# Performance work log

Hardware: AMD Instinct MI355X
Metric: run time of the kernel (lower is better)

## Reference

```python
import jax, jax.numpy as jnp
import numpy as np
import math

DIM = 1024; NH = 16; HD = 64; RANK = 512
E = 8; TOPK = 2; EH = 512
THETA = 10000.0; EPS = 1e-6
B = 2; T = 2048


def setup_inputs():
    key = jax.random.key(0)
    ks = jax.random.split(key, 12)
    s = 0.02
    return {
        "x": jax.random.normal(ks[0], (B, T, DIM), jnp.float32),
        "attn_norm_w": jnp.ones((DIM,), jnp.float32),
        "ffn_norm_w": jnp.ones((DIM,), jnp.float32),
        "q_norm_w": jnp.ones((HD,), jnp.float32),
        "k_norm_w": jnp.ones((HD,), jnp.float32),
        "wq": jax.random.normal(ks[1], (NH * HD, DIM), jnp.float32) * s,
        "wkv_down": jax.random.normal(ks[2], (RANK, DIM), jnp.float32) * s,
        "wkv_up": jax.random.normal(ks[3], (2 * NH * HD, RANK), jnp.float32) * s,
        "wo": jax.random.normal(ks[4], (DIM, NH * HD), jnp.float32) * s,
        "gate_w": jax.random.normal(ks[5], (E, DIM), jnp.float32) * s,
        "shared_w1": jax.random.normal(ks[6], (EH, DIM), jnp.float32) * s,
        "shared_w2": jax.random.normal(ks[7], (DIM, EH), jnp.float32) * s,
        "expert_w1": jax.random.normal(ks[8], (E, EH, DIM), jnp.float32) * s,
        "expert_w2": jax.random.normal(ks[9], (E, DIM, EH), jnp.float32) * s,
    }


def rmsnorm(x, w):
    var = jnp.mean(x * x, axis=-1, keepdims=True)
    return x * jax.lax.rsqrt(var + EPS) * w


def rope(x, cos, sin):
    # x: [B,T,H,HD]; pairs are (even, odd) along last dim. cos/sin: [T,1,HD//2]
    xr = x.reshape(*x.shape[:-1], HD // 2, 2)
    a, b = xr[..., 0], xr[..., 1]
    out = jnp.stack([a * cos - b * sin, a * sin + b * cos], axis=-1)
    return out.reshape(x.shape)


def _block(x, attn_norm_w, ffn_norm_w, q_norm_w, k_norm_w,
           wq, wkv_down, wkv_up, wo, gate_w,
           shared_w1, shared_w2, expert_w1, expert_w2):
    Bb, Tt, C = x.shape
    # ---- MLA attention ----
    h_in = rmsnorm(x, attn_norm_w)
    xq = jnp.einsum('btd,ed->bte', h_in, wq).reshape(Bb, Tt, NH, HD)
    latent = jnp.einsum('btd,rd->btr', h_in, wkv_down)
    kv = jnp.einsum('btr,er->bte', latent, wkv_up).reshape(Bb, Tt, 2, NH, HD)
    xk, xv = kv[:, :, 0], kv[:, :, 1]
    xq = rmsnorm(xq, q_norm_w)
    xk = rmsnorm(xk, k_norm_w)
    # RoPE tables
    inv = 1.0 / (THETA ** (jnp.arange(0, HD, 2, dtype=jnp.float32) / HD))  # [HD/2]
    ang = jnp.arange(Tt, dtype=jnp.float32)[:, None] * inv[None, :]       # [T,HD/2]
    cos = jnp.cos(ang)[:, None, :]
    sin = jnp.sin(ang)[:, None, :]
    xq = rope(xq, cos, sin)
    xk = rope(xk, cos, sin)
    scale = 1.0 / math.sqrt(HD)
    scores = jnp.einsum('bqhd,bkhd->bhqk', xq, xk) * scale
    causal = jnp.tril(jnp.ones((Tt, Tt), dtype=bool))
    scores = jnp.where(causal, scores, jnp.finfo(scores.dtype).min)
    attn = jax.nn.softmax(scores, axis=-1)
    attn_out = jnp.einsum('bhqk,bkhd->bqhd', attn, xv).reshape(Bb, Tt, C)
    attn_out = jnp.einsum('bte,de->btd', attn_out, wo)
    h = x + attn_out  # dropout p=0.0 -> identity

    # ---- DeepSeekMoE ----
    xm = rmsnorm(h, ffn_norm_w).reshape(-1, C)  # [N,D]
    shared = jnp.einsum('nh,dh->nd', jax.nn.silu(jnp.einsum('nd,hd->nh', xm, shared_w1)), shared_w2)
    logits = jnp.einsum('nd,ed->ne', xm, gate_w)
    probs = jax.nn.softmax(logits, axis=-1)
    tkw, tki = jax.lax.top_k(probs, TOPK)
    tkw = tkw / jnp.sum(tkw, axis=-1, keepdims=True)
    aux_loss = jnp.sum(jnp.mean(probs, axis=0) * jnp.mean(logits, axis=0)) * E
    # combine weights per expert: [N,E]
    combine = jnp.einsum('nk,nke->ne', tkw, jax.nn.one_hot(tki, E, dtype=tkw.dtype))
    hidden = jax.nn.silu(jnp.einsum('nd,ehd->neh', xm, expert_w1))  # [N,E,EH]
    yexp = jnp.einsum('neh,edh->ned', hidden, expert_w2)            # [N,E,D]
    routed = jnp.einsum('ne,ned->nd', combine, yexp)
    moe_out = (shared + routed).reshape(Bb, Tt, C)
    out = h + moe_out
    return out, aux_loss


def reference(x, attn_norm_w, ffn_norm_w, q_norm_w, k_norm_w,
              wq, wkv_down, wkv_up, wo, gate_w,
              shared_w1, shared_w2, expert_w1, expert_w2):
    return _block(x, attn_norm_w, ffn_norm_w, q_norm_w, k_norm_w,
                  wq, wkv_down, wkv_up, wo, gate_w,
                  shared_w1, shared_w2, expert_w1, expert_w2)
```

## Files before the change

kernel.cpp:

```cpp
#include <hip/hip_runtime.h>
#include <math.h>

#define DIMC 1024
#define NHEADS 16
#define HDC 64
#define RANKC 512
#define NEXP 8
#define EHC 512
#define SEQC 2048
#define NBATCH 2
#define NTOK (NBATCH * SEQC)
#define EPSF 1e-6f

typedef unsigned short u16;
using bf16x8 = __attribute__((ext_vector_type(8))) short;
using f32x4 = __attribute__((ext_vector_type(4))) float;

__device__ inline u16 f2bf(float f) {
    unsigned int u = __float_as_uint(f);
    u += 0x7fff + ((u >> 16) & 1);
    return (u16)(u >> 16);
}
__device__ inline float bf2f(u16 u) { return __uint_as_float(((unsigned int)u) << 16); }

__device__ inline void gld16(const void* g, void* l) {
    __builtin_amdgcn_global_load_lds(
        (const __attribute__((address_space(1))) unsigned int*)g,
        (__attribute__((address_space(3))) unsigned int*)l, 16, 0, 0);
}

__global__ __launch_bounds__(256) void convall_k(
    const float* __restrict__ wq, const float* __restrict__ wkvd,
    const float* __restrict__ wkvu, const float* __restrict__ wo,
    const float* __restrict__ sw1, const float* __restrict__ sw2,
    const float* __restrict__ ew1, const float* __restrict__ ew2,
    u16* __restrict__ wqkvd_h, u16* __restrict__ wqkvd_l,
    u16* __restrict__ wkvu_h, u16* __restrict__ wkvu_l,
    u16* __restrict__ wo_h, u16* __restrict__ wo_l,
    u16* __restrict__ sw1_b, u16* __restrict__ sw2_b,
    u16* __restrict__ ew1_b, u16* __restrict__ ew2_b,
    const float* __restrict__ x, const float* __restrict__ attn_nw,
    u16* __restrict__ hin_h, u16* __restrict__ hin_l) {
    __shared__ float sred[4];
    if (blockIdx.x >= 12800) {
        int row = blockIdx.x - 12800;
        const float* xr = x + (size_t)row * DIMC;
        int base = threadIdx.x * 4;
        float4 xv = *(const float4*)(xr + base);
        float ss = xv.x * xv.x + xv.y * xv.y + xv.z * xv.z + xv.w * xv.w;
#pragma unroll
        for (int off = 32; off; off >>= 1) ss += __shfl_down(ss, off);
        int wid = threadIdx.x >> 6, lane = threadIdx.x & 63;
        if (lane == 0) sred[wid] = ss;
        __syncthreads();
        float tot = sred[0] + sred[1] + sred[2] + sred[3];
        float sc = rsqrtf(tot * (1.0f / DIMC) + EPSF);
        float4 wv = *(const float4*)(attn_nw + base);
        float o0 = xv.x * sc * wv.x, o1 = xv.y * sc * wv.y;
        float o2 = xv.z * sc * wv.z, o3 = xv.w * sc * wv.w;
        ushort4 h = make_ushort4(f2bf(o0), f2bf(o1), f2bf(o2), f2bf(o3));
        size_t ob = (size_t)row * DIMC + base;
        *(ushort4*)(hin_h + ob) = h;
        ushort4 lo = make_ushort4(f2bf(o0 - bf2f(h.x)), f2bf(o1 - bf2f(h.y)),
                                  f2bf(o2 - bf2f(h.z)), f2bf(o3 - bf2f(h.w)));
        *(ushort4*)(hin_l + ob) = lo;
        return;
    }
    size_t f = ((size_t)blockIdx.x * 256 + threadIdx.x) * 4;
    const float* src;
    u16* dh;
    u16* dl = nullptr;
    size_t local;
    if (f < 1048576) { src = wq; dh = wqkvd_h; dl = wqkvd_l; local = f; }
    else if (f < 1572864) { src = wkvd; dh = wqkvd_h + 1048576; dl = wqkvd_l + 1048576; local = f - 1048576; }
    else if (f < 2621440) { src = wkvu; dh = wkvu_h; dl = wkvu_l; local = f - 1572864; }
    else if (f < 3670016) { src = wo; dh = wo_h; dl = wo_l; local = f - 2621440; }
    else if (f < 4194304) { src = sw1; dh = sw1_b; local = f - 3670016; }
    else if (f < 4718592) { src = sw2; dh = sw2_b; local = f - 4194304; }
    else if (f < 8912896) { src = ew1; dh = ew1_b; local = f - 4718592; }
    else { src = ew2; dh = ew2_b; local = f - 8912896; }
    float4 a = *(const float4*)(src + local);
    ushort4 h = make_ushort4(f2bf(a.x), f2bf(a.y), f2bf(a.z), f2bf(a.w));
    *(ushort4*)(dh + local) = h;
    if (dl) {
        ushort4 lo = make_ushort4(f2bf(a.x - bf2f(h.x)), f2bf(a.y - bf2f(h.y)),
                                  f2bf(a.z - bf2f(h.z)), f2bf(a.w - bf2f(h.w)));
        *(ushort4*)(dl + local) = lo;
    }
}

__global__ __launch_bounds__(256) void rmsnorm_gate_k(const float* __restrict__ x,
                                                      const float* __restrict__ w,
                                                      u16* __restrict__ oh,
                                                      const float* __restrict__ gw,
                                                      float* __restrict__ topw,
                                                      int* __restrict__ topi,
                                                      float* __restrict__ plbuf) {
    int row = blockIdx.x;
    const float* xr = x + (size_t)row * DIMC;
    int base = threadIdx.x * 4;
    float4 xv = *(const float4*)(xr + base);
    float ss = xv.x * xv.x + xv.y * xv.y + xv.z * xv.z + xv.w * xv.w;
#pragma unroll
    for (int off = 32; off; off >>= 1) ss += __shfl_down(ss, off);
    __shared__ float sred[4];
    __shared__ float red[4][NEXP];
    int wid = threadIdx.x >> 6, lane = threadIdx.x & 63;
    if (lane == 0) sred[wid] = ss;
    __syncthreads();
    float tot = sred[0] + sred[1] + sred[2] + sred[3];
    float sc = rsqrtf(tot * (1.0f / DIMC) + EPSF);
    float4 wv = *(const float4*)(w + base);
    float o0 = xv.x * sc * wv.x, o1 = xv.y * sc * wv.y;
    float o2 = xv.z * sc * wv.z, o3 = xv.w * sc * wv.w;
    size_t ob = (size_t)row * DIMC + base;
    *(ushort4*)(oh + ob) = make_ushort4(f2bf(o0), f2bf(o1), f2bf(o2), f2bf(o3));
    float acc[NEXP];
#pragma unroll
    for (int e = 0; e < NEXP; e++) {
        float4 gv = *(const float4*)(gw + (size_t)e * DIMC + base);
        acc[e] = o0 * gv.x + o1 * gv.y + o2 * gv.z + o3 * gv.w;
    }
#pragma unroll
    for (int off = 32; off; off >>= 1)
#pragma unroll
        for (int e = 0; e < NEXP; e++) acc[e] += __shfl_down(acc[e], off);
    if (lane == 0)
#pragma unroll
        for (int e = 0; e < NEXP; e++) red[wid][e] = acc[e];
    __syncthreads();
    if (threadIdx.x == 0) {
        float lg[NEXP], p[NEXP];
        float mx = -1e30f;
#pragma unroll
        for (int e = 0; e < NEXP; e++) {
            lg[e] = red[0][e] + red[1][e] + red[2][e] + red[3][e];
            mx = fmaxf(mx, lg[e]);
        }
        float s = 0.f;
#pragma unroll
        for (int e = 0; e < NEXP; e++) { p[e] = __expf(lg[e] - mx); s += p[e]; }
        float invs = 1.0f / s;
#pragma unroll
        for (int e = 0; e < NEXP; e++) p[e] *= invs;
        int i0 = 0;
        for (int e = 1; e < NEXP; e++) if (p[e] > p[i0]) i0 = e;
        int i1 = (i0 == 0) ? 1 : 0;
        for (int e = 0; e < NEXP; e++) if (e != i0 && p[e] > p[i1]) i1 = e;
        float w0 = p[i0], w1 = p[i1];
        float invw = 1.0f / (w0 + w1);
        topw[row * 2] = w0 * invw;
        topw[row * 2 + 1] = w1 * invw;
        topi[row * 2] = i0;
        topi[row * 2 + 1] = i1;
#pragma unroll
        for (int e = 0; e < NEXP; e++) {
            plbuf[(size_t)e * NTOK + row] = p[e];
            plbuf[(size_t)(NEXP + e) * NTOK + row] = lg[e];
        }
    }
}

template <int EPI>
__global__ __launch_bounds__(256) void gemm_sp(const u16* __restrict__ Ah,
                                               const u16* __restrict__ Al,
                                               const u16* __restrict__ Bh,
                                               const u16* __restrict__ Bl,
                                               float* __restrict__ Cf,
                                               u16* __restrict__ Ch,
                                               u16* __restrict__ Cl,
                                               const float* __restrict__ res,
                                               int M, int K) {
    __shared__ u16 AsH[128 * 64], AsL[128 * 64];
    __shared__ u16 BsH[64 * 64], BsL[64 * 64];
    int m0 = blockIdx.x * 64, n0 = blockIdx.y * 128;
    int t = threadIdx.x;
    int w = t >> 6, l = t & 63;
    int wr = w >> 1, wc = w & 1;
    f32x4 acc[4][2];
#pragma unroll
    for (int i = 0; i < 4; i++)
#pragma unroll
        for (int j = 0; j < 2; j++) acc[i][j] = {0.f, 0.f, 0.f, 0.f};
    int lr = t >> 2, lcb = (t & 3) * 8;
    size_t aoff = (size_t)(n0 + lr) * K + lcb;
    size_t boff = (size_t)(m0 + lr) * K + lcb;
    u16* lAH = AsH + t * 8;
    u16* lAL = AsL + t * 8;
    u16* lBH = BsH + t * 8;
    u16* lBL = BsL + t * 8;
    int arow = l & 15, kblk = (l >> 4) * 8;
    for (int k0 = 0; k0 < K; k0 += 64) {
        if (k0) __syncthreads();
        gld16(Ah + aoff + k0, lAH);
        gld16(Ah + aoff + k0 + (size_t)64 * K, lAH + 2048);
        gld16(Ah + aoff + k0 + 32, lAH + 4096);
        gld16(Ah + aoff + k0 + 32 + (size_t)64 * K, lAH + 6144);
        gld16(Al + aoff + k0, lAL);
        gld16(Al + aoff + k0 + (size_t)64 * K, lAL + 2048);
        gld16(Al + aoff + k0 + 32, lAL + 4096);
        gld16(Al + aoff + k0 + 32 + (size_t)64 * K, lAL + 6144);
        gld16(Bh + boff + k0, lBH);
        gld16(Bh + boff + k0 + 32, lBH + 2048);
        gld16(Bl + boff + k0, lBL);
        gld16(Bl + boff + k0 + 32, lBL + 2048);
        __syncthreads();
#pragma unroll
        for (int c = 0; c < 2; c++) {
            int ab = c * 4096, bb = c * 2048;
            bf16x8 ah[4], al[4], bh[2], bl[2];
#pragma unroll
            for (int i = 0; i < 4; i++) {
                int ar = ab + (wr * 64 + i * 16 + arow) * 32 + kblk;
                ah[i] = *(bf16x8*)(AsH + ar);
                al[i] = *(bf16x8*)(AsL + ar);
            }
#pragma unroll
            for (int j = 0; j < 2; j++) {
                int br = bb + (wc * 32 + j * 16 + arow) * 32 + kblk;
                bh[j] = *(bf16x8*)(BsH + br);
                bl[j] = *(bf16x8*)(BsL + br);
            }
#pragma unroll
            for (int i = 0; i < 4; i++)
#pragma unroll
                for (int j = 0; j < 2; j++) {
                    acc[i][j] = __builtin_amdgcn_mfma_f32_16x16x32_bf16(ah[i], bh[j], acc[i][j], 0, 0, 0);
                    acc[i][j] = __builtin_amdgcn_mfma_f32_16x16x32_bf16(ah[i], bl[j], acc[i][j], 0, 0, 0);
                    acc[i][j] = __builtin_amdgcn_mfma_f32_16x16x32_bf16(al[i], bh[j], acc[i][j], 0, 0, 0);
                }
        }
    }
    int crow = (l >> 4) * 4, ccol = l & 15;
#pragma unroll
    for (int i = 0; i < 4; i++) {
#pragma unroll
        for (int r = 0; r < 4; r++) {
            int n = n0 + wr * 64 + i * 16 + crow + r;
#pragma unroll
            for (int j = 0; j < 2; j++) {
                int mc = m0 + wc * 32 + j * 16 + ccol;
                float vv = acc[i][j][r];
                if (EPI == 0 || EPI == 1) {
                    size_t idx = (size_t)n * M + mc;
                    if (EPI == 1) vv += res[idx];
                    Cf[idx] = vv;
                } else {
                    if (mc < 1024) {
                        Cf[(size_t)n * 1024 + mc] = vv;
                    } else {
                        size_t idx = (size_t)n * 512 + (mc - 1024);
                        u16 hi = f2bf(vv);
                        Ch[idx] = hi;
                        Cl[idx] = f2bf(vv - bf2f(hi));
                    }
                }
            }
        }
    }
}

__global__ __launch_bounds__(256) void gemm_fin(const u16* __restrict__ A,
                                                const u16* __restrict__ B,
                                                float* __restrict__ Cf,
                                                const float* __restrict__ res,
                                                const u16* __restrict__ yx,
                                                const float* __restrict__ tw,
                                                const float* __restrict__ sums,
                                                int M, int K) {
    if (blockIdx.y == 32) {
        if (blockIdx.x == 0 && threadIdx.x == 0) {
            const float invN = 1.0f / NTOK;
            float a = 0;
            for (int e = 0; e < NEXP; e++) a += (sums[e] * invN) * (sums[NEXP + e] * invN);
            Cf[(size_t)4194304] = a * NEXP;
        }
        return;
    }
    __shared__ u16 As[128 * 64];
    __shared__ u16 Bs[64 * 64];
    int m0 = blockIdx.x * 64, n0 = blockIdx.y * 128;
    int t = threadIdx.x;
    int w = t >> 6, l = t & 63;
    int wr = w >> 1, wc = w & 1;
    f32x4 acc[4][2];
#pragma unroll
    for (int i = 0; i < 4; i++)
#pragma unroll
        for (int j = 0; j < 2; j++) acc[i][j] = {0.f, 0.f, 0.f, 0.f};
    int lr = t >> 2, lcb = (t & 3) * 8;
    const u16* ga = A + (size_t)(n0 + lr) * K + lcb;
    const u16* gb = B + (size_t)(m0 + lr) * K + lcb;
    u16* lA = As + t * 8;
    u16* lB = Bs + t * 8;
    int arow = l & 15, kblk = (l >> 4) * 8;
    for (int k0 = 0; k0 < K; k0 += 64) {
        if (k0) __syncthreads();
        gld16(ga + k0, lA);
        gld16(ga + k0 + (size_t)64 * K, lA + 2048);
        gld16(ga + k0 + 32, lA + 4096);
        gld16(ga + k0 + 32 + (size_t)64 * K, lA + 6144);
        gld16(gb + k0, lB);
        gld16(gb + k0 + 32, lB + 2048);
        __syncthreads();
#pragma unroll
        for (int c = 0; c < 2; c++) {
            int ab = c * 4096, bb = c * 2048;
            bf16x8 af[4], bfr[2];
#pragma unroll
            for (int i = 0; i < 4; i++)
                af[i] = *(bf16x8*)(As + ab + (wr * 64 + i * 16 + arow) * 32 + kblk);
#pragma unroll
            for (int j = 0; j < 2; j++)
                bfr[j] = *(bf16x8*)(Bs + bb + (wc * 32 + j * 16 + arow) * 32 + kblk);
#pragma unroll
            for (int i = 0; i < 4; i++)
#pragma unroll
                for (int j = 0; j < 2; j++)
                    acc[i][j] = __builtin_amdgcn_mfma_f32_16x16x32_bf16(af[i], bfr[j], acc[i][j], 0, 0, 0);
        }
    }
    int crow = (l >> 4) * 4, ccol = l & 15;
#pragma unroll
    for (int i = 0; i < 4; i++) {
#pragma unroll
        for (int r = 0; r < 4; r++) {
            int n = n0 + wr * 64 + i * 16 + crow + r;
#pragma unroll
            for (int j = 0; j < 2; j++) {
                int mc = m0 + wc * 32 + j * 16 + ccol;
                size_t idx = (size_t)n * M + mc;
                float y0 = bf2f(yx[(size_t)(2 * n) * 1024 + mc]);
                float y1 = bf2f(yx[(size_t)(2 * n + 1) * 1024 + mc]);
                Cf[idx] = acc[i][j][r] + res[idx] + tw[2 * n] * y0 + tw[2 * n + 1] * y1;
            }
        }
    }
}

__global__ __launch_bounds__(256) void qknorm_rope_k(const float* __restrict__ q,
                                                     const float* __restrict__ kv,
                                                     const float* __restrict__ qw,
                                                     const float* __restrict__ kw,
                                                     u16* __restrict__ qhi, u16* __restrict__ qlo,
                                                     u16* __restrict__ khi, u16* __restrict__ klo) {
    int bid = blockIdx.x * 4 + (threadIdx.x >> 6);
    int head = bid & (NHEADS - 1);
    int n = bid >> 4;
    int pos = n & (SEQC - 1);
    int lane = threadIdx.x & 63;
    int i = lane >> 1;
    float inv = powf(10000.0f, -(float)(2 * i) * (1.0f / HDC));
    float ang = (float)pos * inv;
    float cs = cosf(ang), sn = sinf(ang);
    size_t off = (size_t)n * DIMC + head * HDC + lane;
    {
        float v = q[off];
        float ss = v * v;
#pragma unroll
        for (int o2 = 32; o2; o2 >>= 1) ss += __shfl_down(ss, o2);
        ss = __shfl(ss, 0);
        float sc = rsqrtf(ss * (1.0f / HDC) + EPSF);
        v = v * sc * qw[lane];
        float partner = __shfl_xor(v, 1);
        float outv = (lane & 1) ? (partner * sn + v * cs) : (v * cs - partner * sn);
        outv *= 0.125f;
        u16 hi = f2bf(outv);
        qhi[off] = hi;
        qlo[off] = f2bf(outv - bf2f(hi));
    }
    {
        float v = kv[(size_t)n * 2048 + head * HDC + lane];
        float ss = v * v;
#pragma unroll
        for (int o2 = 32; o2; o2 >>= 1) ss += __shfl_down(ss, o2);
        ss = __shfl(ss, 0);
        float sc = rsqrtf(ss * (1.0f / HDC) + EPSF);
        v = v * sc * kw[lane];
        float partner = __shfl_xor(v, 1);
        float outv = (lane & 1) ? (partner * sn + v * cs) : (v * cs - partner * sn);
        u16 hi = f2bf(outv);
        khi[off] = hi;
        klo[off] = f2bf(outv - bf2f(hi));
    }
}

__global__ __launch_bounds__(256) void transp_k(const float* __restrict__ kv,
                                                u16* __restrict__ vthi,
                                                u16* __restrict__ vtlo) {
    __shared__ float T[64][68];
    int j0 = blockIdx.x * 64, head = blockIdx.y, b = blockIdx.z;
    int t = threadIdx.x;
    int jr = t >> 2, c0 = (t & 3) * 16;
    const float* src = kv + ((size_t)(b * SEQC + j0 + jr)) * 2048 + 1024 + head * HDC + c0;
#pragma unroll
    for (int u = 0; u < 4; u++) {
        float4 v4 = *(const float4*)(src + u * 4);
        T[c0 + u * 4 + 0][jr] = v4.x;
        T[c0 + u * 4 + 1][jr] = v4.y;
        T[c0 + u * 4 + 2][jr] = v4.z;
        T[c0 + u * 4 + 3][jr] = v4.w;
    }
    __syncthreads();
    int d = t >> 2, jb = (t & 3) * 16;
    size_t obase = ((size_t)((b * NHEADS + head) * HDC + d)) * SEQC + j0 + jb;
#pragma unroll
    for (int u = 0; u < 4; u++) {
        float f0 = T[d][jb + u * 4 + 0], f1 = T[d][jb + u * 4 + 1];
        float f2 = T[d][jb + u * 4 + 2], f3 = T[d][jb + u * 4 + 3];
        ushort4 h = make_ushort4(f2bf(f0), f2bf(f1), f2bf(f2), f2bf(f3));
        ushort4 lo = make_ushort4(f2bf(f0 - bf2f(h.x)), f2bf(f1 - bf2f(h.y)),
                                  f2bf(f2 - bf2f(h.z)), f2bf(f3 - bf2f(h.w)));
        *(ushort4*)(vthi + obase + u * 4) = h;
        *(ushort4*)(vtlo + obase + u * 4) = lo;
    }
}

__device__ __forceinline__ void attn_tile(const bf16x8 (&qh)[2], const bf16x8 (&ql)[2],
                                          f32x4 (&O)[4], float (&mrow)[4], float (&lrow)[4],
                                          const u16* KHs, const u16* KLs,
                                          const u16* VHs, const u16* VLs,
                                          u16* myPH, u16* myPL,
                                          int la, int lg, int w, bool diag) {
    f32x4 S[4];
    __builtin_amdgcn_s_setprio(1);
#pragma unroll
    for (int ct = 0; ct < 4; ct++) {
        int row = ct * 16 + la;
        int sw = (row & 7) << 4;
        int a0 = ((row << 7) + (lg << 4)) ^ sw;
        int a1 = ((row << 7) + 64 + (lg << 4)) ^ sw;
        bf16x8 kh0 = *(const bf16x8*)((const char*)KHs + a0);
        bf16x8 kh1 = *(const bf16x8*)((const char*)KHs + a1);
        bf16x8 kl0 = *(const bf16x8*)((const char*)KLs + a0);
        bf16x8 kl1 = *(const bf16x8*)((const char*)KLs + a1);
        f32x4 s = {0.f, 0.f, 0.f, 0.f};
        s = __builtin_amdgcn_mfma_f32_16x16x32_bf16(qh[0], kh0, s, 0, 0, 0);
        s = __builtin_amdgcn_mfma_f32_16x16x32_bf16(qh[1], kh1, s, 0, 0, 0);
        s = __builtin_amdgcn_mfma_f32_16x16x32_bf16(qh[0], kl0, s, 0, 0, 0);
        s = __builtin_amdgcn_mfma_f32_16x16x32_bf16(qh[1], kl1, s, 0, 0, 0);
        s = __builtin_amdgcn_mfma_f32_16x16x32_bf16(ql[0], kh0, s, 0, 0, 0);
        s = __builtin_amdgcn_mfma_f32_16x16x32_bf16(ql[1], kh1, s, 0, 0, 0);
        S[ct] = s;
    }
    __builtin_amdgcn_s_setprio(0);
    if (diag) {
#pragma unroll
        for (int ct = 0; ct < 4; ct++)
#pragma unroll
            for (int r = 0; r < 4; r++)
                if (ct * 16 + la > w * 16 + lg * 4 + r) S[ct][r] = -1e30f;
    }
    float rmax[4], rsum[4];
#pragma unroll
    for (int r = 0; r < 4; r++)
        rmax[r] = fmaxf(fmaxf(S[0][r], S[1][r]), fmaxf(S[2][r], S[3][r]));
#pragma unroll
    for (int off = 1; off < 16; off <<= 1)
#pragma unroll
        for (int r = 0; r < 4; r++) rmax[r] = fmaxf(rmax[r], __shfl_xor(rmax[r], off));
    float corr[4];
#pragma unroll
    for (int r = 0; r < 4; r++) {
        float mn = fmaxf(mrow[r], rmax[r]);
        corr[r] = __expf(mrow[r] - mn);
        mrow[r] = mn;
        rsum[r] = 0.f;
    }
#pragma unroll
    for (int ct = 0; ct < 4; ct++) {
#pragma unroll
        for (int r = 0; r < 4; r++) {
            float p = __expf(S[ct][r] - mrow[r]);
            rsum[r] += p;
            u16 hi = f2bf(p);
            int pidx = (lg * 4 + r) * 68 + ct * 16 + la;
            myPH[pidx] = hi;
            myPL[pidx] = f2bf(p - bf2f(hi));
        }
    }
#pragma unroll
    for (int off = 1; off < 16; off <<= 1)
#pragma unroll
        for (int r = 0; r < 4; r++) rsum[r] += __shfl_xor(rsum[r], off);
#pragma unroll
    for (int r = 0; r < 4; r++) lrow[r] = lrow[r] * corr[r] + rsum[r];
#pragma unroll
    for (int ct = 0; ct < 4; ct++)
#pragma unroll
        for (int r = 0; r < 4; r++) O[ct][r] *= corr[r];
    asm volatile("s_waitcnt lgkmcnt(0)" ::: "memory");
    __builtin_amdgcn_sched_barrier(0);
    bf16x8 pa0 = *(const bf16x8*)(myPH + la * 68 + lg * 8);
    bf16x8 pa1 = *(const bf16x8*)(myPH + la * 68 + 32 + lg * 8);
    bf16x8 pl0 = *(const bf16x8*)(myPL + la * 68 + lg * 8);
    bf16x8 pl1 = *(const bf16x8*)(myPL + la * 68 + 32 + lg * 8);
    __builtin_amdgcn_s_setprio(1);
#pragma unroll
    for (int ct = 0; ct < 4; ct++) {
        int row = ct * 16 + la;
        int sw = (row & 7) << 4;
        int a0 = ((row << 7) + (lg << 4)) ^ sw;
        int a1 = ((row << 7) + 64 + (lg << 4)) ^ sw;
        bf16x8 vh0 = *(const bf16x8*)((const char*)VHs + a0);
        bf16x8 vh1 = *(const bf16x8*)((const char*)VHs + a1);
        bf16x8 vl0 = *(const bf16x8*)((const char*)VLs + a0);
        bf16x8 vl1 = *(const bf16x8*)((const char*)VLs + a1);
        f32x4 o = O[ct];
        o = __builtin_amdgcn_mfma_f32_16x16x32_bf16(pa0, vh0, o, 0, 0, 0);
        o = __builtin_amdgcn_mfma_f32_16x16x32_bf16(pa1, vh1, o, 0, 0, 0);
        o = __builtin_amdgcn_mfma_f32_16x16x32_bf16(pl0, vh0, o, 0, 0, 0);
        o = __builtin_amdgcn_mfma_f32_16x16x32_bf16(pl1, vh1, o, 0, 0, 0);
        o = __builtin_amdgcn_mfma_f32_16x16x32_bf16(pa0, vl0, o, 0, 0, 0);
        o = __builtin_amdgcn_mfma_f32_16x16x32_bf16(pa1, vl1, o, 0, 0, 0);
        O[ct] = o;
    }
    __builtin_amdgcn_s_setprio(0);
}

__global__ __launch_bounds__(256) void flash_k(const u16* __restrict__ qhi,
                                               const u16* __restrict__ qlo,
                                               const u16* __restrict__ khi,
                                               const u16* __restrict__ klo,
                                               const u16* __restrict__ vthi,
                                               const u16* __restrict__ vtlo,
                                               u16* __restrict__ aoh,
                                               u16* __restrict__ aol) {
    __shared__ u16 KHs[4096], KLs[4096], VHs[4096], VLs[4096];
    __shared__ u16 PH[4][16 * 68], PL[4][16 * 68];
    int id = blockIdx.x;
    int xcd = id & 7, slot = id >> 3;
    int grp = ((slot >> 4) << 3) | xcd;
    int pr = slot & 15;
    int head = grp & 15, b = grp >> 4;
    int qtA = pr, qtB = 31 - pr;
    int t = threadIdx.x, w = t >> 6, l = t & 63;
    int la = l & 15, lg = l >> 4;
    size_t qoffA = ((size_t)(b * SEQC + qtA * 64 + w * 16 + la)) * DIMC + head * HDC;
    size_t qoffB = ((size_t)(b * SEQC + qtB * 64 + w * 16 + la)) * DIMC + head * HDC;
    bf16x8 qhA[2], qlA[2], qhB[2], qlB[2];
    qhA[0] = *(const bf16x8*)(qhi + qoffA + lg * 8);
    qhA[1] = *(const bf16x8*)(qhi + qoffA + 32 + lg * 8);
    qlA[0] = *(const bf16x8*)(qlo + qoffA + lg * 8);
    qlA[1] = *(const bf16x8*)(qlo + qoffA + 32 + lg * 8);
    qhB[0] = *(const bf16x8*)(qhi + qoffB + lg * 8);
    qhB[1] = *(const bf16x8*)(qhi + qoffB + 32 + lg * 8);
    qlB[0] = *(const bf16x8*)(qlo + qoffB + lg * 8);
    qlB[1] = *(const bf16x8*)(qlo + qoffB + 32 + lg * 8);
    int d0 = t * 16, d1 = 4096 + t * 16;
    int s0 = d0 ^ (((d0 >> 7) & 7) << 4);
    int s1 = d1 ^ (((d1 >> 7) & 7) << 4);
    int r0 = (s0 >> 7) & 63, ir0 = s0 & 127;
    int r1 = (s1 >> 7) & 63, ir1 = s1 & 127;
    size_t kb0 = ((size_t)(b * SEQC + r0) * DIMC + head * HDC) * 2 + ir0;
    size_t kb1 = ((size_t)(b * SEQC + r1) * DIMC + head * HDC) * 2 + ir1;
    size_t vb0 = ((size_t)((b * NHEADS + head) * HDC + r0)) * SEQC * 2 + ir0;
    size_t vb1 = ((size_t)((b * NHEADS + head) * HDC + r1)) * SEQC * 2 + ir1;
    const char* khp = (const char*)khi;
    const char* klp = (const char*)klo;
    const char* vhp = (const char*)vthi;
    const char* vlp = (const char*)vtlo;
    f32x4 OA[4], OB[4];
#pragma unroll
    for (int ct = 0; ct < 4; ct++) {
        OA[ct] = {0.f, 0.f, 0.f, 0.f};
        OB[ct] = {0.f, 0.f, 0.f, 0.f};
    }
    float mA[4] = {-1e30f, -1e30f, -1e30f, -1e30f};
    float lA[4] = {0.f, 0.f, 0.f, 0.f};
    float mB[4] = {-1e30f, -1e30f, -1e30f, -1e30f};
    float lB[4] = {0.f, 0.f, 0.f, 0.f};
    u16* myPH = PH[w];
    u16* myPL = PL[w];
    for (int kt = 0; kt <= qtB; kt++) {
        __syncthreads();
        size_t ko = (size_t)kt * (64 * DIMC * 2);
        size_t vo = (size_t)kt * 128;
        gld16(khp + kb0 + ko, KHs + t * 8);
        gld16(khp + kb1 + ko, KHs + t * 8 + 2048);
        gld16(klp + kb0 + ko, KLs + t * 8);
        gld16(klp + kb1 + ko, KLs + t * 8 + 2048);
        gld16(vhp + vb0 + vo, VHs + t * 8);
        gld16(vhp + vb1 + vo, VHs + t * 8 + 2048);
        gld16(vlp + vb0 + vo, VLs + t * 8);
        gld16(vlp + vb1 + vo, VLs + t * 8 + 2048);
        __syncthreads();
        attn_tile(qhB, qlB, OB, mB, lB, KHs, KLs, VHs, VLs, myPH, myPL, la, lg, w, kt == qtB);
        if (kt <= qtA)
            attn_tile(qhA, qlA, OA, mA, lA, KHs, KLs, VHs, VLs, myPH, myPL, la, lg, w, kt == qtA);
    }
    size_t obA = ((size_t)(b * SEQC + qtA * 64 + w * 16 + lg * 4)) * DIMC + head * HDC;
    size_t obB = ((size_t)(b * SEQC + qtB * 64 + w * 16 + lg * 4)) * DIMC + head * HDC;
#pragma unroll
    for (int ct = 0; ct < 4; ct++) {
#pragma unroll
        for (int r = 0; r < 4; r++) {
            float va = OA[ct][r] / lA[r];
            size_t ia = obA + (size_t)r * DIMC + ct * 16 + la;
            u16 ha = f2bf(va);
            aoh[ia] = ha;
            aol[ia] = f2bf(va - bf2f(ha));
            float vb = OB[ct][r] / lB[r];
            size_t ib = obB + (size_t)r * DIMC + ct * 16 + la;
            u16 hb = f2bf(vb);
            aoh[ib] = hb;
            aol[ib] = f2bf(vb - bf2f(hb));
        }
    }
}

__global__ __launch_bounds__(256) void auxroute_k(const float* __restrict__ plbuf,
                                                  float* __restrict__ sums,
                                                  const int* __restrict__ topi,
                                                  int* __restrict__ cnt,
                                                  int* __restrict__ perm) {
    __shared__ float red[4];
    __shared__ int lcnt[NEXP];
    if (blockIdx.x < 16) {
        int col = blockIdx.x;
        const float* src = plbuf + (size_t)col * NTOK;
        float s = 0.f;
#pragma unroll
        for (int i = 0; i < NTOK / 256; i++) s += src[threadIdx.x + i * 256];
#pragma unroll
        for (int off = 32; off; off >>= 1) s += __shfl_down(s, off);
        int wid = threadIdx.x >> 6, lane = threadIdx.x & 63;
        if (lane == 0) red[wid] = s;
        __syncthreads();
        if (threadIdx.x == 0) sums[col] = red[0] + red[1] + red[2] + red[3];
        return;
    }
    if (threadIdx.x < NEXP) lcnt[threadIdx.x] = 0;
    __syncthreads();
    for (int i = 0; i < NTOK / 256; i++) {
        int n = i * 256 + threadIdx.x;
#pragma unroll
        for (int kk = 0; kk < 2; kk++) {
            int slot = n * 2 + kk;
            int e = topi[slot];
            int pos = atomicAdd(&lcnt[e], 1);
            perm[e * 4096 + pos] = slot;
        }
    }
    __syncthreads();
    if (threadIdx.x < NEXP) cnt[threadIdx.x] = lcnt[threadIdx.x];
}

__global__ __launch_bounds__(256) void moe_h_k(const u16* __restrict__ xb,
                                               const u16* __restrict__ w1,
                                               const u16* __restrict__ sw1b,
                                               const int* __restrict__ perm,
                                               const int* __restrict__ cnt,
                                               u16* __restrict__ hid,
                                               u16* __restrict__ s1b) {
    int e = blockIdx.z;
    bool shared = (e == NEXP);
    int count = shared ? NTOK : cnt[e];
    int n0 = blockIdx.y * 128;
    if (n0 >= count) return;
    int m0 = blockIdx.x * 64;
    __shared__ u16 As[128 * 64];
    __shared__ u16 Bs[64 * 64];
    int t = threadIdx.x;
    int w = t >> 6, l = t & 63;
    int wr = w >> 1, wc = w & 1;
    f32x4 acc[4][2];
#pragma unroll
    for (int i = 0; i < 4; i++)
#pragma unroll
        for (int j = 0; j < 2; j++) acc[i][j] = {0.f, 0.f, 0.f, 0.f};
    int lr = t >> 2, lcb = (t & 3) * 8;
    int tok0, tok1;
    if (shared) {
        tok0 = n0 + lr;
        tok1 = n0 + lr + 64;
    } else {
        tok0 = perm[e * 4096 + min(n0 + lr, count - 1)] >> 1;
        tok1 = perm[e * 4096 + min(n0 + lr + 64, count - 1)] >> 1;
    }
    const u16* ga0 = xb + (size_t)tok0 * DIMC + lcb;
    const u16* ga1 = xb + (size_t)tok1 * DIMC + lcb;
    const u16* gb = (shared ? sw1b : w1 + (size_t)e * EHC * DIMC) + (size_t)(m0 + lr) * DIMC + lcb;
    u16* lA = As + t * 8;
    u16* lB = Bs + t * 8;
    int arow = l & 15, kblk = (l >> 4) * 8;
    for (int k0 = 0; k0 < DIMC; k0 += 64) {
        if (k0) __syncthreads();
        gld16(ga0 + k0, lA);
        gld16(ga1 + k0, lA + 2048);
        gld16(ga0 + k0 + 32, lA + 4096);
        gld16(ga1 + k0 + 32, lA + 6144);
        gld16(gb + k0, lB);
        gld16(gb + k0 + 32, lB + 2048);
        __syncthreads();
#pragma unroll
        for (int c = 0; c < 2; c++) {
            int ab = c * 4096, bb = c * 2048;
            bf16x8 af[4], bfr[2];
#pragma unroll
            for (int i = 0; i < 4; i++)
                af[i] = *(bf16x8*)(As + ab + (wr * 64 + i * 16 + arow) * 32 + kblk);
#pragma unroll
            for (int j = 0; j < 2; j++)
                bfr[j] = *(bf16x8*)(Bs + bb + (wc * 32 + j * 16 + arow) * 32 + kblk);
#pragma unroll
            for (int i = 0; i < 4; i++)
#pragma unroll
                for (int j = 0; j < 2; j++)
                    acc[i][j] = __builtin_amdgcn_mfma_f32_16x16x32_bf16(af[i], bfr[j], acc[i][j], 0, 0, 0);
        }
    }
    int crow = (l >> 4) * 4, ccol = l & 15;
#pragma unroll
    for (int i = 0; i < 4; i++) {
#pragma unroll
        for (int r = 0; r < 4; r++) {
            int hrow = n0 + wr * 64 + i * 16 + crow + r;
            if (hrow >= count) continue;
            size_t dstrow = shared ? (size_t)hrow : (size_t)perm[e * 4096 + hrow];
            u16* dst = shared ? s1b : hid;
#pragma unroll
            for (int j = 0; j < 2; j++) {
                int mc = m0 + wc * 32 + j * 16 + ccol;
                float vv = acc[i][j][r];
                vv = vv / (1.0f + __expf(-vv));
                dst[dstrow * EHC + mc] = f2bf(vv);
            }
        }
    }
}

__global__ __launch_bounds__(256) void moe_c_k(const u16* __restrict__ hid,
                                               const u16* __restrict__ w2,
                                               const int* __restrict__ perm,
                                               const int* __restrict__ cnt,
                                               u16* __restrict__ yexp) {
    int e = blockIdx.z;
    int count = cnt[e];
    int n0 = blockIdx.y * 128;
    if (n0 >= count) return;
    int m0 = blockIdx.x * 64;
    __shared__ u16 As[128 * 64];
    __shared__ u16 Bs[64 * 64];
    int t = threadIdx.x;
    int w = t >> 6, l = t & 63;
    int wr = w >> 1, wc = w & 1;
    f32x4 acc[4][2];
#pragma unroll
    for (int i = 0; i < 4; i++)
#pragma unroll
        for (int j = 0; j < 2; j++) acc[i][j] = {0.f, 0.f, 0.f, 0.f};
    int lr = t >> 2, lcb = (t & 3) * 8;
    int slot0 = perm[e * 4096 + min(n0 + lr, count - 1)];
    int slot1 = perm[e * 4096 + min(n0 + lr + 64, count - 1)];
    const u16* ga0 = hid + (size_t)slot0 * EHC + lcb;
    const u16* ga1 = hid + (size_t)slot1 * EHC + lcb;
    const u16* gb = w2 + (size_t)e * DIMC * EHC + (size_t)(m0 + lr) * EHC + lcb;
    u16* lA = As + t * 8;
    u16* lB = Bs + t * 8;
    int arow = l & 15, kblk = (l >> 4) * 8;
    for (int k0 = 0; k0 < EHC; k0 += 64) {
        if (k0) __syncthreads();
        gld16(ga0 + k0, lA);
        gld16(ga1 + k0, lA + 2048);
        gld16(ga0 + k0 + 32, lA + 4096);
        gld16(ga1 + k0 + 32, lA + 6144);
        gld16(gb + k0, lB);
        gld16(gb + k0 + 32, lB + 2048);
        __syncthreads();
#pragma unroll
        for (int c = 0; c < 2; c++) {
            int ab = c * 4096, bb = c * 2048;
            bf16x8 af[4], bfr[2];
#pragma unroll
            for (int i = 0; i < 4; i++)
                af[i] = *(bf16x8*)(As + ab + (wr * 64 + i * 16 + arow) * 32 + kblk);
#pragma unroll
            for (int j = 0; j < 2; j++)
                bfr[j] = *(bf16x8*)(Bs + bb + (wc * 32 + j * 16 + arow) * 32 + kblk);
#pragma unroll
            for (int i = 0; i < 4; i++)
#pragma unroll
                for (int j = 0; j < 2; j++)
                    acc[i][j] = __builtin_amdgcn_mfma_f32_16x16x32_bf16(af[i], bfr[j], acc[i][j], 0, 0, 0);
        }
    }
    int crow = (l >> 4) * 4, ccol = l & 15;
#pragma unroll
    for (int i = 0; i < 4; i++) {
#pragma unroll
        for (int r = 0; r < 4; r++) {
            int pos = n0 + wr * 64 + i * 16 + crow + r;
            if (pos >= count) continue;
            int slot = perm[e * 4096 + pos];
#pragma unroll
            for (int j = 0; j < 2; j++) {
                int mc = m0 + wc * 32 + j * 16 + ccol;
                yexp[(size_t)slot * 1024 + mc] = f2bf(acc[i][j][r]);
            }
        }
    }
}

extern "C" void kernel_launch(void* const* d_in, const int* in_sizes, int n_in,
                              void* d_out, int out_size, void* d_ws, size_t ws_size,
                              hipStream_t stream) {
    const float* x = (const float*)d_in[0];
    const float* attn_nw = (const float*)d_in[1];
    const float* ffn_nw = (const float*)d_in[2];
    const float* q_nw = (const float*)d_in[3];
    const float* k_nw = (const float*)d_in[4];
    const float* wq = (const float*)d_in[5];
    const float* wkv_down = (const float*)d_in[6];
    const float* wkv_up = (const float*)d_in[7];
    const float* wo = (const float*)d_in[8];
    const float* gate_w = (const float*)d_in[9];
    const float* sw1 = (const float*)d_in[10];
    const float* sw2 = (const float*)d_in[11];
    const float* ew1 = (const float*)d_in[12];
    const float* ew2 = (const float*)d_in[13];
    float* out = (float*)d_out;
    char* W = (char*)d_ws;
    const size_t MB = (size_t)1 << 20;

    u16* wqkvd_h = (u16*)(W + 0 * MB);
    u16* wqkvd_l = (u16*)(W + 3 * MB);
    u16* wkvu_h = (u16*)(W + 6 * MB);
    u16* wkvu_l = (u16*)(W + 8 * MB);
    u16* wo_h = (u16*)(W + 10 * MB);
    u16* wo_l = (u16*)(W + 12 * MB);
    u16* sw1_b = (u16*)(W + 14 * MB);
    u16* sw2_b = (u16*)(W + 15 * MB);
    u16* ew1_b = (u16*)(W + 16 * MB);
    u16* ew2_b = (u16*)(W + 24 * MB);
    u16* hin_h = (u16*)(W + 32 * MB);
    u16* hin_l = (u16*)(W + 40 * MB);
    float* qf = (float*)(W + 48 * MB);
    float* kvf = (float*)(W + 64 * MB);
    u16* lat_h = (u16*)(W + 96 * MB);
    u16* lat_l = (u16*)(W + 100 * MB);
    u16* qhi = (u16*)(W + 104 * MB);
    u16* qlo = (u16*)(W + 112 * MB);
    u16* khi = (u16*)(W + 120 * MB);
    u16* klo = (u16*)(W + 128 * MB);
    u16* vthi = (u16*)(W + 136 * MB);
    u16* vtlo = (u16*)(W + 144 * MB);
    float* sums = (float*)(W + 152 * MB);
    int* cnt = (int*)(W + 152 * MB + 256);
    float* topw = (float*)(W + 152 * MB + 4096);
    int* topi = (int*)(W + 152 * MB + 4096 + 32768);
    int* perm = (int*)(W + 152 * MB + 4096 + 65536);
    float* plbuf = (float*)(W + 153 * MB);
    u16* ao_h = hin_h;
    u16* ao_l = hin_l;
    u16* xm_b = (u16*)qf;
    float* h = (float*)(W + 64 * MB);
    u16* s1_b = lat_h;
    u16* hid = qhi;
    u16* yexp = qlo;

    convall_k<<<16896, 256, 0, stream>>>(wq, wkv_down, wkv_up, wo, sw1, sw2, ew1, ew2,
                                         wqkvd_h, wqkvd_l, wkvu_h, wkvu_l,
                                         wo_h, wo_l, sw1_b, sw2_b, ew1_b, ew2_b,
                                         x, attn_nw, hin_h, hin_l);

    gemm_sp<5><<<dim3(24, 32), 256, 0, stream>>>(hin_h, hin_l, wqkvd_h, wqkvd_l, qf, lat_h, lat_l, nullptr, 1024, DIMC);
    gemm_sp<0><<<dim3(32, 32), 256, 0, stream>>>(lat_h, lat_l, wkvu_h, wkvu_l, kvf, nullptr, nullptr, nullptr, 2048, RANKC);
    qknorm_rope_k<<<NTOK * NHEADS / 4, 256, 0, stream>>>(qf, kvf, q_nw, k_nw, qhi, qlo, khi, klo);
    transp_k<<<dim3(SEQC / 64, NHEADS, NBATCH), 256, 0, stream>>>(kvf, vthi, vtlo);
    flash_k<<<dim3(512), 256, 0, stream>>>(qhi, qlo, khi, klo, vthi, vtlo, ao_h, ao_l);
    gemm_sp<1><<<dim3(16, 32), 256, 0, stream>>>(ao_h, ao_l, wo_h, wo_l, h, nullptr, nullptr, x, DIMC, DIMC);
    rmsnorm_gate_k<<<NTOK, 256, 0, stream>>>(h, ffn_nw, xm_b, gate_w, topw, topi, plbuf);
    auxroute_k<<<17, 256, 0, stream>>>(plbuf, sums, topi, cnt, perm);
    moe_h_k<<<dim3(8, 32, 9), 256, 0, stream>>>(xm_b, ew1_b, sw1_b, perm, cnt, hid, s1_b);
    moe_c_k<<<dim3(16, 32, 8), 256, 0, stream>>>(hid, ew2_b, perm, cnt, yexp);
    gemm_fin<<<dim3(16, 33), 256, 0, stream>>>(s1_b, sw2_b, out, h, yexp, topw, sums, DIMC, EHC);
}
```

Before: 397.2 us.

## Register-prefetch next K/V tile in flash attention instead of direct LDS loads

Replaces the direct global-to-LDS loads of K/V hi/lo tiles with a register prefetch. The next tile is loaded into registers while the current tile is computed, then stored to LDS at the start of the next iteration. This aims to hide global memory latency behind the attention MFMA work. It also adds launch_bounds min-blocks of 2, which caps registers; the extra 8 float4 registers per thread risk spills or lower occupancy.

```diff
diff --git a/kernel.cpp b/kernel.cpp
--- a/kernel.cpp
+++ b/kernel.cpp
@@ -518,14 +518,14 @@
     __builtin_amdgcn_s_setprio(0);
 }
 
-__global__ __launch_bounds__(256) void flash_k(const u16* __restrict__ qhi,
-                                               const u16* __restrict__ qlo,
-                                               const u16* __restrict__ khi,
-                                               const u16* __restrict__ klo,
-                                               const u16* __restrict__ vthi,
-                                               const u16* __restrict__ vtlo,
-                                               u16* __restrict__ aoh,
-                                               u16* __restrict__ aol) {
+__global__ __launch_bounds__(256, 2) void flash_k(const u16* __restrict__ qhi,
+                                                  const u16* __restrict__ qlo,
+                                                  const u16* __restrict__ khi,
+                                                  const u16* __restrict__ klo,
+                                                  const u16* __restrict__ vthi,
+                                                  const u16* __restrict__ vtlo,
+                                                  u16* __restrict__ aoh,
+                                                  u16* __restrict__ aol) {
     __shared__ u16 KHs[4096], KLs[4096], VHs[4096], VLs[4096];
     __shared__ u16 PH[4][16 * 68], PL[4][16 * 68];
     int id = blockIdx.x;
@@ -572,18 +572,43 @@
     float lB[4] = {0.f, 0.f, 0.f, 0.f};
     u16* myPH = PH[w];
     u16* myPL = PL[w];
+    char* dKH = (char*)KHs + 16 * t;
+    char* dKL = (char*)KLs + 16 * t;
+    char* dVH = (char*)VHs + 16 * t;
+    char* dVL = (char*)VLs + 16 * t;
+    float4 rv[8];
+    {
+        rv[0] = *(const float4*)(khp + kb0);
+        rv[1] = *(const float4*)(khp + kb1);
+        rv[2] = *(const float4*)(klp + kb0);
+        rv[3] = *(const float4*)(klp + kb1);
+        rv[4] = *(const float4*)(vhp + vb0);
+        rv[5] = *(const float4*)(vhp + vb1);
+        rv[6] = *(const float4*)(vlp + vb0);
+        rv[7] = *(const float4*)(vlp + vb1);
+    }
     for (int kt = 0; kt <= qtB; kt++) {
         __syncthreads();
-        size_t ko = (size_t)kt * (64 * DIMC * 2);
-        size_t vo = (size_t)kt * 128;
-        gld16(khp + kb0 + ko, KHs + t * 8);
-        gld16(khp + kb1 + ko, KHs + t * 8 + 2048);
-        gld16(klp + kb0 + ko, KLs + t * 8);
-        gld16(klp + kb1 + ko, KLs + t * 8 + 2048);
-        gld16(vhp + vb0 + vo, VHs + t * 8);
-        gld16(vhp + vb1 + vo, VHs + t * 8 + 2048);
-        gld16(vlp + vb0 + vo, VLs + t * 8);
-        gld16(vlp + vb1 + vo, VLs + t * 8 + 2048);
+        *(float4*)(dKH) = rv[0];
+        *(float4*)(dKH + 4096) = rv[1];
+        *(float4*)(dKL) = rv[2];
+        *(float4*)(dKL + 4096) = rv[3];
+        *(float4*)(dVH) = rv[4];
+        *(float4*)(dVH + 4096) = rv[5];
+        *(float4*)(dVL) = rv[6];
+        *(float4*)(dVL + 4096) = rv[7];
+        if (kt < qtB) {
+            size_t ko = (size_t)(kt + 1) * (64 * DIMC * 2);
+            size_t vo = (size_t)(kt + 1) * 128;
+            rv[0] = *(const float4*)(khp + kb0 + ko);
+            rv[1] = *(const float4*)(khp + kb1 + ko);
+            rv[2] = *(const float4*)(klp + kb0 + ko);
+            rv[3] = *(const float4*)(klp + kb1 + ko);
+            rv[4] = *(const float4*)(vhp + vb0 + vo);
+            rv[5] = *(const float4*)(vhp + vb1 + vo);
+            rv[6] = *(const float4*)(vlp + vb0 + vo);
+            rv[7] = *(const float4*)(vlp + vb1 + vo);
+        }
         __syncthreads();
         attn_tile(qhB, qlB, OB, mB, lB, KHs, KLs, VHs, VLs, myPH, myPL, la, lg, w, kt == qtB);
         if (kt <= qtA)
```

Measured after the change: 450.9 us. +13.5%, slower.
